# Kernel optimization log

Measured on AMD Instinct MI355X. Metric: run time of the kernel, lower is better.

## Reference

```python
import jax, jax.numpy as jnp
import numpy as np

# Static DAG configuration (mirrors GraphState): 1 input node + L layers of K nodes.
L = 8          # depth layers (well under t_budget=12)
K = 8          # nodes per layer
D = 128        # node hidden width (node.D)
B = 4096       # batch size
INDEG = 4      # in-edges per non-input node
N = 1 + L * K  # total nodes


def _build_graph():
    """Deterministic static edge lists: srcs[l][k, j] = parent node id (topologically earlier)."""
    rng = np.random.default_rng(0)
    srcs = []
    n_prev = 1  # node 0 is the INPUT node
    for _ in range(L):
        srcs.append(rng.integers(0, n_prev, size=(K, INDEG)))
        n_prev += K
    return srcs


def setup_inputs() -> dict:
    key = jax.random.key(0)
    k1, k2, k3 = jax.random.split(key, 3)
    X = jax.random.normal(k1, (B, D), dtype=jnp.float32)
    # scale ~ sqrt(2/(indeg*D)) to keep relu activations O(1) over 8 layers
    W = jax.random.normal(k2, (N, D, D), dtype=jnp.float32) * 0.06
    b = jax.random.normal(k3, (N, D), dtype=jnp.float32) * 0.01
    return {"X_batch": X, "W_all": W, "bias_all": b}


def reference(X_batch, W_all, bias_all):
    srcs = _build_graph()  # static python/numpy index constants -> jit-friendly
    # INPUT node (id 0): input_dim == D so no zero-padding; V_out = relu(X W^T + b)
    v0 = jax.nn.relu(X_batch @ W_all[0].T + bias_all[0])          # (B, D)
    outs = v0[None]                                               # (n_done, B, D)
    node = 1
    for l in range(L):
        idx = srcs[l]                                             # (K, INDEG) static
        V_in = outs[idx].sum(axis=1)                              # inbox gather-sum -> (K, B, D)
        Wl = W_all[node:node + K]                                 # (K, D, D)
        bl = bias_all[node:node + K]                              # (K, D)
        V_weighted = jnp.einsum('kbd,ked->kbe', V_in, Wl) + bl[:, None, :]
        V_out = jax.nn.relu(V_weighted)                           # apply_primitive(relu)
        outs = jnp.concatenate([outs, V_out], axis=0)
        node += K
    # output nodes = last layer; final = mean over fired output nodes
    return outs[-K:].mean(axis=0)                                 # (B, D)
```

## Files before the change

### kernel.cpp

```cpp
#include <hip/hip_runtime.h>
#include <cstdint>
#include <cstring>

#define BATCH   4096
#define DIM     128
#define NLAYERS 8
#define KNODES  8
#define NDEG    4
#define NNODES  65
#define NODE_ELEMS (BATCH * DIM)
#define ROWS    16
#define SLOTS   35
#define TILE_B  (ROWS * 256)
#define NTHREADS 512

typedef float    f32x4 __attribute__((ext_vector_type(4)));
typedef short    s16x8 __attribute__((ext_vector_type(8)));
typedef uint32_t u32x4 __attribute__((ext_vector_type(4)));

struct LayerSrcs { int p[KNODES][NDEG]; };

struct Sched {
  uint64_t pinfo[NLAYERS * KNODES];
  int8_t   dst[NLAYERS * KNODES];
  int8_t   root_dst;
};

__device__ __forceinline__ float bf_lo(uint32_t u) {
  union { uint32_t i; float f; } x; x.i = u << 16; return x.f;
}
__device__ __forceinline__ float bf_hi(uint32_t u) {
  union { uint32_t i; float f; } x; x.i = u & 0xffff0000u; return x.f;
}
__device__ __forceinline__ uint32_t f2bf(float f) {
  union { float f; uint32_t i; } x; x.f = f;
  return (x.i + 0x7fffu + ((x.i >> 16) & 1u)) >> 16;
}
__device__ __forceinline__ uint32_t pack2(float a, float b) {
  return f2bf(a) | (f2bf(b) << 16);
}

__global__ __launch_bounds__(256)
void pack_w(const float* __restrict__ W, uint16_t* __restrict__ Wp) {
  int gid  = blockIdx.x * 256 + threadIdx.x;
  int lane = gid & 63;
  int n    = (gid >> 6) & 7;
  int ks   = (gid >> 9) & 3;
  int node = gid >> 11;
  int col  = n * 16 + (lane & 15);
  int k0   = ks * 32 + (lane >> 4) * 8;
  const float* src = W + ((size_t)node * DIM + col) * DIM + k0;
  f32x4 v0 = *(const f32x4*)src;
  f32x4 v1 = *(const f32x4*)(src + 4);
  u32x4 pk;
  pk.x = pack2(v0.x, v0.y); pk.y = pack2(v0.z, v0.w);
  pk.z = pack2(v1.x, v1.y); pk.w = pack2(v1.z, v1.w);
  *(u32x4*)(Wp + (size_t)gid * 8) = pk;
}

__device__ __forceinline__ void gemm_node(
    char* lds, int sbuf, int n, int dstv,
    const uint16_t* __restrict__ Wp, const float* __restrict__ bias,
    uint16_t* __restrict__ outs, float* macc,
    int row0, int lane, int w, int lr, int lg)
{
  if (dstv == -3) return;
  const char* sb = lds + (size_t)(SLOTS + sbuf) * TILE_B;
  s16x8 af[4], wf[4];
#pragma unroll
  for (int ks = 0; ks < 4; ++ks) {
    af[ks] = *(const s16x8*)(sb + ((lr * 256 + ks * 64 + lg * 16) ^ ((lr & 7) << 4)));
    wf[ks] = *(const s16x8*)(Wp + ((((size_t)n * 4 + ks) * 8 + w) << 9) + lane * 8);
  }
  f32x4 acc = (f32x4){0.f, 0.f, 0.f, 0.f};
#pragma unroll
  for (int ks = 0; ks < 4; ++ks)
    acc = __builtin_amdgcn_mfma_f32_16x16x32_bf16(af[ks], wf[ks], acc, 0, 0, 0);

  const int col = w * 16 + lr;
  const float bv = bias[(size_t)n * DIM + col];
  if (dstv >= 0) {
    char* db = lds + (size_t)dstv * TILE_B;
#pragma unroll
    for (int j = 0; j < 4; ++j) {
      int row = lg * 4 + j;
      float v = fmaxf(acc[j] + bv, 0.f);
      *(uint16_t*)(db + ((row * 256 + col * 2) ^ ((row & 7) << 4))) = (uint16_t)f2bf(v);
    }
  } else if (dstv == -1) {
    uint16_t* gb = outs + (size_t)n * NODE_ELEMS + (size_t)row0 * DIM + col;
#pragma unroll
    for (int j = 0; j < 4; ++j) {
      int row = lg * 4 + j;
      float v = fmaxf(acc[j] + bv, 0.f);
      gb[(size_t)row * DIM] = (uint16_t)f2bf(v);
      gb += 0;
    }
  } else {
#pragma unroll
    for (int j = 0; j < 4; ++j)
      macc[j] += 0.125f * fmaxf(acc[j] + bv, 0.f);
  }
}


__device__ __forceinline__ void gemm_node2(
    char* lds, int sbuf, int n, int dstv,
    const uint16_t* __restrict__ Wp, const float* __restrict__ bias,
    uint16_t* __restrict__ outs, float* macc,
    int row0, int lane, int w, int lr, int lg)
{
  if (dstv == -3) return;
  const char* sb = lds + (size_t)(SLOTS + sbuf) * TILE_B;
  s16x8 af[4], wf[4];
#pragma unroll
  for (int ks = 0; ks < 4; ++ks) {
    af[ks] = *(const s16x8*)(sb + ((lr * 256 + ks * 64 + lg * 16) ^ ((lr & 7) << 4)));
    wf[ks] = *(const s16x8*)(Wp + ((((size_t)n * 4 + ks) * 8 + w) << 9) + lane * 8);
  }
  f32x4 acc = (f32x4){0.f, 0.f, 0.f, 0.f};
#pragma unroll
  for (int ks = 0; ks < 4; ++ks)
    acc = __builtin_amdgcn_mfma_f32_16x16x32_bf16(af[ks], wf[ks], acc, 0, 0, 0);

  const int col = w * 16 + lr;
  const float bv = bias[(size_t)n * DIM + col];
  if (dstv >= 0) {
    char* db = lds + (size_t)dstv * TILE_B;
#pragma unroll
    for (int j = 0; j < 4; ++j) {
      int row = lg * 4 + j;
      float v = fmaxf(acc[j] + bv, 0.f);
      *(uint16_t*)(db + ((row * 256 + col * 2) ^ ((row & 7) << 4))) = (uint16_t)f2bf(v);
    }
  } else if (dstv == -1) {
    uint16_t* gb = outs + (size_t)n * NODE_ELEMS + (size_t)row0 * DIM + col;
#pragma unroll
    for (int j = 0; j < 4; ++j) {
      int row = lg * 4 + j;
      float v = fmaxf(acc[j] + bv, 0.f);
      gb[(size_t)row * DIM] = (uint16_t)f2bf(v);
    }
  } else {
#pragma unroll
    for (int j = 0; j < 4; ++j)
      macc[j] += 0.125f * fmaxf(acc[j] + bv, 0.f);
  }
}

__global__ __launch_bounds__(NTHREADS)
void dag_exec(const float* __restrict__ X, const uint16_t* __restrict__ Wp,
              const float* __restrict__ bias, uint16_t* __restrict__ outs,
              float* __restrict__ out, Sched sch)
{
  __shared__ char lds[(SLOTS + 4) * TILE_B];
  const int t    = threadIdx.x;
  const int lane = t & 63;
  const int w    = t >> 6;
  const int lr   = lane & 15;
  const int lg   = lane >> 4;
  const int row0 = blockIdx.x * ROWS;

  float macc[4] = {0.f, 0.f, 0.f, 0.f};

  if (t < ROWS * 16) {
    int r = t >> 4, c = t & 15;
    const float* xp = X + (size_t)(row0 + r) * DIM + c * 8;
    f32x4 v0 = *(const f32x4*)xp;
    f32x4 v1 = *(const f32x4*)(xp + 4);
    u32x4 pk;
    pk.x = pack2(v0.x, v0.y); pk.y = pack2(v0.z, v0.w);
    pk.z = pack2(v1.x, v1.y); pk.w = pack2(v1.z, v1.w);
    int off = (r * 256 + c * 16) ^ ((r & 7) << 4);
    *(u32x4*)(lds + (size_t)SLOTS * TILE_B + off) = pk;
  }
  __syncthreads();
  gemm_node2(lds, 0, 0, sch.root_dst, Wp, bias, outs, macc, row0, lane, w, lr, lg);
  __syncthreads();

  for (int l = 0; l < NLAYERS; ++l) {
#pragma unroll
    for (int h = 0; h < 2; ++h) {
      const int k0 = h * 4;
      const uint64_t pi0 = sch.pinfo[l * KNODES + k0 + 0];
      const uint64_t pi1 = sch.pinfo[l * KNODES + k0 + 1];
      const uint64_t pi2 = sch.pinfo[l * KNODES + k0 + 2];
      const uint64_t pi3 = sch.pinfo[l * KNODES + k0 + 3];
      const int d0 = sch.dst[l * KNODES + k0 + 0];
      const int d1 = sch.dst[l * KNODES + k0 + 1];
      const int d2 = sch.dst[l * KNODES + k0 + 2];
      const int d3 = sch.dst[l * KNODES + k0 + 3];

#pragma unroll
      for (int it = 0; it < 2; ++it) {
        const int lin = it * NTHREADS + t;
        const int nk  = lin >> 8;
        const uint64_t pinfo = (nk < 2) ? (nk == 0 ? pi0 : pi1) : (nk == 2 ? pi2 : pi3);
        const int dv         = (nk < 2) ? (nk == 0 ? d0 : d1) : (nk == 2 ? d2 : d3);
        if (dv != -3) {
          const int r = (lin >> 4) & 15, c = lin & 15;
          const int linoff = r * 256 + (c << 4);
          const int soff   = linoff ^ ((r & 7) << 4);
          float s0 = 0, s1 = 0, s2 = 0, s3 = 0, s4 = 0, s5 = 0, s6 = 0, s7 = 0;
#pragma unroll
          for (int p = 0; p < NDEG; ++p) {
            const int e  = (int)((pinfo >> (p * 16)) & 0xffff);
            const int ps = (e & 0xff) - 1;
            u32x4 v;
            if (ps >= 0) {
              v = *(const u32x4*)(lds + (size_t)ps * TILE_B + soff);
            } else {
              const int pid = e >> 8;
              v = *(const u32x4*)((const char*)(outs + (size_t)pid * NODE_ELEMS +
                                                (size_t)row0 * DIM) + linoff);
            }
            s0 += bf_lo(v.x); s1 += bf_hi(v.x);
            s2 += bf_lo(v.y); s3 += bf_hi(v.y);
            s4 += bf_lo(v.z); s5 += bf_hi(v.z);
            s6 += bf_lo(v.w); s7 += bf_hi(v.w);
          }
          u32x4 pk;
          pk.x = pack2(s0, s1); pk.y = pack2(s2, s3);
          pk.z = pack2(s4, s5); pk.w = pack2(s6, s7);
          *(u32x4*)(lds + (size_t)(SLOTS + nk) * TILE_B + soff) = pk;
        }
      }
      __syncthreads();

#pragma unroll
      for (int nk = 0; nk < 4; ++nk) {
        const int dv = (nk < 2) ? (nk == 0 ? d0 : d1) : (nk == 2 ? d2 : d3);
        const int n  = 1 + l * KNODES + k0 + nk;
        gemm_node2(lds, nk, n, dv, Wp, bias, outs, macc, row0, lane, w, lr, lg);
      }
      __syncthreads();
    }
  }

  {
    const int col = w * 16 + lr;
#pragma unroll
    for (int j = 0; j < 4; ++j) {
      const int row = lg * 4 + j;
      out[(size_t)(row0 + row) * DIM + col] = macc[j];
    }
  }
}

namespace nprng {
static inline uint32_t hashmix(uint32_t v, uint32_t& hc) {
  v ^= hc; hc *= 0x931e8875u; v *= hc; v ^= v >> 16; return v;
}
static inline uint32_t mixf(uint32_t x, uint32_t y) {
  uint32_t r = x * 0xca01f9ddu - y * 0x4973f715u;
  r ^= r >> 16;
  return r;
}
struct Pcg {
  unsigned __int128 state, inc;
  bool has32; uint32_t saved;
  void step() {
    const unsigned __int128 MUL =
        ((unsigned __int128)2549297995355413924ULL << 64) | 4865540595714422341ULL;
    state = state * MUL + inc;
  }
  void init_seed0() {
    uint32_t pool[4];
    uint32_t hc = 0x43b0d7e5u;
    for (int i = 0; i < 4; ++i) pool[i] = hashmix(0u, hc);
    for (int s = 0; s < 4; ++s)
      for (int d = 0; d < 4; ++d)
        if (s != d) pool[d] = mixf(pool[d], hashmix(pool[s], hc));
    uint32_t st[8];
    uint32_t hb = 0x8b51f9ddu;
    int cyc = 0;
    for (int i = 0; i < 8; ++i) {
      uint32_t dv = pool[cyc]; cyc = (cyc + 1) & 3;
      dv ^= hb; hb *= 0x58f38dedu; dv *= hb; dv ^= dv >> 16;
      st[i] = dv;
    }
    uint64_t v[4];
    for (int i = 0; i < 4; ++i)
      v[i] = (uint64_t)st[2 * i] | ((uint64_t)st[2 * i + 1] << 32);
    unsigned __int128 s128 = ((unsigned __int128)v[0] << 64) | v[1];
    unsigned __int128 i128 = ((unsigned __int128)v[2] << 64) | v[3];
    state = 0; inc = (i128 << 1) | 1;
    step(); state += s128; step();
    has32 = false; saved = 0;
  }
  uint64_t next64() {
    step();
    uint64_t rot = (uint64_t)(state >> 122);
    uint64_t x = (uint64_t)(state >> 64) ^ (uint64_t)state;
    return rot ? ((x >> rot) | (x << (64 - rot))) : x;
  }
  uint32_t next32() {
    if (has32) { has32 = false; return saved; }
    uint64_t v = next64();
    has32 = true; saved = (uint32_t)(v >> 32);
    return (uint32_t)v;
  }
  uint32_t lemire32(uint32_t rng_incl) {
    uint32_t rng_excl = rng_incl + 1u;
    uint64_t m = (uint64_t)next32() * (uint64_t)rng_excl;
    uint32_t leftover = (uint32_t)m;
    if (leftover < rng_excl) {
      uint32_t threshold = (0xFFFFFFFFu - rng_incl) % rng_excl;
      while (leftover < threshold) {
        m = (uint64_t)next32() * (uint64_t)rng_excl;
        leftover = (uint32_t)m;
      }
    }
    return (uint32_t)(m >> 32);
  }
};
}

extern "C" void kernel_launch(void* const* d_in, const int* in_sizes, int n_in,
                              void* d_out, int out_size, void* d_ws, size_t ws_size,
                              hipStream_t stream) {
  const float* X    = (const float*)d_in[0];
  const float* W    = (const float*)d_in[1];
  const float* bias = (const float*)d_in[2];
  float* out        = (float*)d_out;

  uint16_t* Wp   = (uint16_t*)d_ws;
  uint16_t* outs = (uint16_t*)((char*)d_ws + (size_t)NNODES * DIM * DIM * 2);

  nprng::Pcg rng; rng.init_seed0();
  LayerSrcs srcs[NLAYERS];
  int n_prev = 1;
  for (int l = 0; l < NLAYERS; ++l) {
    for (int k = 0; k < KNODES; ++k)
      for (int j = 0; j < NDEG; ++j)
        srcs[l].p[k][j] = (n_prev == 1) ? 0 : (int)rng.lemire32((uint32_t)(n_prev - 1));
    n_prev += KNODES;
  }

  bool alive[NNODES];
  for (int i = 0; i < NNODES; ++i) alive[i] = false;
  for (int i = NNODES - KNODES; i < NNODES; ++i) alive[i] = true;
  for (int l = NLAYERS - 1; l >= 0; --l)
    for (int k = 0; k < KNODES; ++k)
      if (alive[1 + l * KNODES + k])
        for (int j = 0; j < NDEG; ++j) alive[srcs[l].p[k][j]] = true;

  int last_use[NNODES];
  for (int i = 0; i < NNODES; ++i) last_use[i] = -1;
  for (int l = 0; l < NLAYERS; ++l)
    for (int k = 0; k < KNODES; ++k)
      if (alive[1 + l * KNODES + k])
        for (int j = 0; j < NDEG; ++j) {
          int s = srcs[l].p[k][j];
          if (l > last_use[s]) last_use[s] = l;
        }

  int slot_of[NNODES];
  for (int i = 0; i < NNODES; ++i) slot_of[i] = -1;
  int freeStk[SLOTS], nfree = 0;
  for (int i = SLOTS - 1; i >= 0; --i) freeStk[nfree++] = i;

  Sched sch;
  slot_of[0] = freeStk[--nfree];
  sch.root_dst = (int8_t)slot_of[0];

  for (int l = 0; l < NLAYERS; ++l) {
    for (int k = 0; k < KNODES; ++k) {
      const int node = 1 + l * KNODES + k;
      int dv;
      if (!alive[node])            dv = -3;
      else if (l == NLAYERS - 1)   dv = -2;
      else if (nfree > 0)          dv = slot_of[node] = freeStk[--nfree];
      else                         dv = -1;
      sch.dst[l * KNODES + k] = (int8_t)dv;

      uint64_t w64 = 0;
      for (int j = 0; j < NDEG; ++j) {
        const int src = srcs[l].p[k][j];
        const int enc = ((slot_of[src] + 1) & 0xff) | (src << 8);
        w64 |= (uint64_t)enc << (j * 16);
      }
      sch.pinfo[l * KNODES + k] = w64;
    }
    for (int n = 0; n < NNODES; ++n)
      if (slot_of[n] >= 0 && last_use[n] == l) {
        freeStk[nfree++] = slot_of[n];
        slot_of[n] = -1;
      }
  }

  pack_w<<<dim3(520), dim3(256), 0, stream>>>(W, Wp);
  dag_exec<<<dim3(BATCH / ROWS), dim3(NTHREADS), 0, stream>>>(X, Wp, bias, outs, out, sch);
}
```

Measured before the change: 125.6 us.

## Replace inbox gather-sum with per-parent MFMA accumulation, one wave pair per node

Each layer now assigns one pair of waves to each of the 8 nodes (1024 threads) and computes all nodes of a layer concurrently. Instead of summing the parent activations into a bf16 staging buffer before the GEMM, each parent fragment is fed directly into MFMA, so the summation happens in the fp32 accumulator. This removes the staging buffers and one barrier per half-layer, and the root GEMM reads X straight into registers. The cost is 4x the MFMA count, more threads competing for registers, and LDS atomics for the output mean.

```diff
diff --git a/kernel.cpp b/kernel.cpp
--- a/kernel.cpp
+++ b/kernel.cpp
@@ -10,9 +10,9 @@
 #define NNODES  65
 #define NODE_ELEMS (BATCH * DIM)
 #define ROWS    16
-#define SLOTS   35
+#define SLOTS   37
 #define TILE_B  (ROWS * 256)
-#define NTHREADS 512
+#define NTHREADS 1024
 
 typedef float    f32x4 __attribute__((ext_vector_type(4)));
 typedef short    s16x8 __attribute__((ext_vector_type(8)));
@@ -26,12 +26,6 @@
   int8_t   root_dst;
 };
 
-__device__ __forceinline__ float bf_lo(uint32_t u) {
-  union { uint32_t i; float f; } x; x.i = u << 16; return x.f;
-}
-__device__ __forceinline__ float bf_hi(uint32_t u) {
-  union { uint32_t i; float f; } x; x.i = u & 0xffff0000u; return x.f;
-}
 __device__ __forceinline__ uint32_t f2bf(float f) {
   union { float f; uint32_t i; } x; x.f = f;
   return (x.i + 0x7fffu + ((x.i >> 16) & 1u)) >> 16;
@@ -58,192 +52,137 @@
   *(u32x4*)(Wp + (size_t)gid * 8) = pk;
 }
 
-__device__ __forceinline__ void gemm_node(
-    char* lds, int sbuf, int n, int dstv,
-    const uint16_t* __restrict__ Wp, const float* __restrict__ bias,
-    uint16_t* __restrict__ outs, float* macc,
-    int row0, int lane, int w, int lr, int lg)
-{
-  if (dstv == -3) return;
-  const char* sb = lds + (size_t)(SLOTS + sbuf) * TILE_B;
-  s16x8 af[4], wf[4];
-#pragma unroll
-  for (int ks = 0; ks < 4; ++ks) {
-    af[ks] = *(const s16x8*)(sb + ((lr * 256 + ks * 64 + lg * 16) ^ ((lr & 7) << 4)));
-    wf[ks] = *(const s16x8*)(Wp + ((((size_t)n * 4 + ks) * 8 + w) << 9) + lane * 8);
-  }
-  f32x4 acc = (f32x4){0.f, 0.f, 0.f, 0.f};
-#pragma unroll
-  for (int ks = 0; ks < 4; ++ks)
-    acc = __builtin_amdgcn_mfma_f32_16x16x32_bf16(af[ks], wf[ks], acc, 0, 0, 0);
-
-  const int col = w * 16 + lr;
-  const float bv = bias[(size_t)n * DIM + col];
-  if (dstv >= 0) {
-    char* db = lds + (size_t)dstv * TILE_B;
-#pragma unroll
-    for (int j = 0; j < 4; ++j) {
-      int row = lg * 4 + j;
-      float v = fmaxf(acc[j] + bv, 0.f);
-      *(uint16_t*)(db + ((row * 256 + col * 2) ^ ((row & 7) << 4))) = (uint16_t)f2bf(v);
-    }
-  } else if (dstv == -1) {
-    uint16_t* gb = outs + (size_t)n * NODE_ELEMS + (size_t)row0 * DIM + col;
-#pragma unroll
-    for (int j = 0; j < 4; ++j) {
-      int row = lg * 4 + j;
-      float v = fmaxf(acc[j] + bv, 0.f);
-      gb[(size_t)row * DIM] = (uint16_t)f2bf(v);
-      gb += 0;
-    }
-  } else {
-#pragma unroll
-    for (int j = 0; j < 4; ++j)
-      macc[j] += 0.125f * fmaxf(acc[j] + bv, 0.f);
-  }
-}
-
-
-__device__ __forceinline__ void gemm_node2(
-    char* lds, int sbuf, int n, int dstv,
-    const uint16_t* __restrict__ Wp, const float* __restrict__ bias,
-    uint16_t* __restrict__ outs, float* macc,
-    int row0, int lane, int w, int lr, int lg)
-{
-  if (dstv == -3) return;
-  const char* sb = lds + (size_t)(SLOTS + sbuf) * TILE_B;
-  s16x8 af[4], wf[4];
-#pragma unroll
-  for (int ks = 0; ks < 4; ++ks) {
-    af[ks] = *(const s16x8*)(sb + ((lr * 256 + ks * 64 + lg * 16) ^ ((lr & 7) << 4)));
-    wf[ks] = *(const s16x8*)(Wp + ((((size_t)n * 4 + ks) * 8 + w) << 9) + lane * 8);
-  }
-  f32x4 acc = (f32x4){0.f, 0.f, 0.f, 0.f};
-#pragma unroll
-  for (int ks = 0; ks < 4; ++ks)
-    acc = __builtin_amdgcn_mfma_f32_16x16x32_bf16(af[ks], wf[ks], acc, 0, 0, 0);
-
-  const int col = w * 16 + lr;
-  const float bv = bias[(size_t)n * DIM + col];
-  if (dstv >= 0) {
-    char* db = lds + (size_t)dstv * TILE_B;
-#pragma unroll
-    for (int j = 0; j < 4; ++j) {
-      int row = lg * 4 + j;
-      float v = fmaxf(acc[j] + bv, 0.f);
-      *(uint16_t*)(db + ((row * 256 + col * 2) ^ ((row & 7) << 4))) = (uint16_t)f2bf(v);
-    }
-  } else if (dstv == -1) {
-    uint16_t* gb = outs + (size_t)n * NODE_ELEMS + (size_t)row0 * DIM + col;
-#pragma unroll
-    for (int j = 0; j < 4; ++j) {
-      int row = lg * 4 + j;
-      float v = fmaxf(acc[j] + bv, 0.f);
-      gb[(size_t)row * DIM] = (uint16_t)f2bf(v);
-    }
-  } else {
-#pragma unroll
-    for (int j = 0; j < 4; ++j)
-      macc[j] += 0.125f * fmaxf(acc[j] + bv, 0.f);
-  }
-}
-
 __global__ __launch_bounds__(NTHREADS)
 void dag_exec(const float* __restrict__ X, const uint16_t* __restrict__ Wp,
               const float* __restrict__ bias, uint16_t* __restrict__ outs,
               float* __restrict__ out, Sched sch)
 {
-  __shared__ char lds[(SLOTS + 4) * TILE_B];
+  __shared__ char lds[SLOTS * TILE_B + 2048 * 4];
+  float* mb = (float*)(lds + (size_t)SLOTS * TILE_B);
+
   const int t    = threadIdx.x;
   const int lane = t & 63;
-  const int w    = t >> 6;
+  const int wv   = t >> 6;
   const int lr   = lane & 15;
   const int lg   = lane >> 4;
+  const int kn   = wv & 7;
+  const int h    = wv >> 3;
   const int row0 = blockIdx.x * ROWS;
 
-  float macc[4] = {0.f, 0.f, 0.f, 0.f};
-
-  if (t < ROWS * 16) {
-    int r = t >> 4, c = t & 15;
-    const float* xp = X + (size_t)(row0 + r) * DIM + c * 8;
-    f32x4 v0 = *(const f32x4*)xp;
-    f32x4 v1 = *(const f32x4*)(xp + 4);
-    u32x4 pk;
-    pk.x = pack2(v0.x, v0.y); pk.y = pack2(v0.z, v0.w);
-    pk.z = pack2(v1.x, v1.y); pk.w = pack2(v1.z, v1.w);
-    int off = (r * 256 + c * 16) ^ ((r & 7) << 4);
-    *(u32x4*)(lds + (size_t)SLOTS * TILE_B + off) = pk;
+  mb[t] = 0.f;
+  mb[t + 1024] = 0.f;
+
+  if (wv < 2) {
+    const int h2 = wv;
+    f32x4 acc[4];
+#pragma unroll
+    for (int n = 0; n < 4; ++n) acc[n] = (f32x4){0.f, 0.f, 0.f, 0.f};
+#pragma unroll
+    for (int ks = 0; ks < 4; ++ks) {
+      const float* xp = X + (size_t)(row0 + lr) * DIM + ks * 32 + lg * 8;
+      f32x4 v0 = *(const f32x4*)xp;
+      f32x4 v1 = *(const f32x4*)(xp + 4);
+      u32x4 pk;
+      pk.x = pack2(v0.x, v0.y); pk.y = pack2(v0.z, v0.w);
+      pk.z = pack2(v1.x, v1.y); pk.w = pack2(v1.z, v1.w);
+      s16x8 af;
+      __builtin_memcpy(&af, &pk, 16);
+#pragma unroll
+      for (int n = 0; n < 4; ++n) {
+        const size_t ci = ((size_t)(0 * 4 + ks) * 8 + h2 * 4 + n);
+        s16x8 wf = *(const s16x8*)(Wp + (ci << 9) + lane * 8);
+        acc[n] = __builtin_amdgcn_mfma_f32_16x16x32_bf16(af, wf, acc[n], 0, 0, 0);
+      }
+    }
+    char* db = lds + (size_t)sch.root_dst * TILE_B;
+#pragma unroll
+    for (int n = 0; n < 4; ++n) {
+      const int col = (h2 * 4 + n) * 16 + lr;
+      const float bv = bias[col];
+#pragma unroll
+      for (int j = 0; j < 4; ++j) {
+        const int row = lg * 4 + j;
+        float v = fmaxf(acc[n][j] + bv, 0.f);
+        *(uint16_t*)(db + ((row * 256 + col * 2) ^ ((row & 7) << 4))) = (uint16_t)f2bf(v);
+      }
+    }
   }
   __syncthreads();
-  gemm_node2(lds, 0, 0, sch.root_dst, Wp, bias, outs, macc, row0, lane, w, lr, lg);
-  __syncthreads();
 
   for (int l = 0; l < NLAYERS; ++l) {
-#pragma unroll
-    for (int h = 0; h < 2; ++h) {
-      const int k0 = h * 4;
-      const uint64_t pi0 = sch.pinfo[l * KNODES + k0 + 0];
-      const uint64_t pi1 = sch.pinfo[l * KNODES + k0 + 1];
-      const uint64_t pi2 = sch.pinfo[l * KNODES + k0 + 2];
-      const uint64_t pi3 = sch.pinfo[l * KNODES + k0 + 3];
-      const int d0 = sch.dst[l * KNODES + k0 + 0];
-      const int d1 = sch.dst[l * KNODES + k0 + 1];
-      const int d2 = sch.dst[l * KNODES + k0 + 2];
-      const int d3 = sch.dst[l * KNODES + k0 + 3];
-
-#pragma unroll
-      for (int it = 0; it < 2; ++it) {
-        const int lin = it * NTHREADS + t;
-        const int nk  = lin >> 8;
-        const uint64_t pinfo = (nk < 2) ? (nk == 0 ? pi0 : pi1) : (nk == 2 ? pi2 : pi3);
-        const int dv         = (nk < 2) ? (nk == 0 ? d0 : d1) : (nk == 2 ? d2 : d3);
-        if (dv != -3) {
-          const int r = (lin >> 4) & 15, c = lin & 15;
-          const int linoff = r * 256 + (c << 4);
-          const int soff   = linoff ^ ((r & 7) << 4);
-          float s0 = 0, s1 = 0, s2 = 0, s3 = 0, s4 = 0, s5 = 0, s6 = 0, s7 = 0;
-#pragma unroll
-          for (int p = 0; p < NDEG; ++p) {
-            const int e  = (int)((pinfo >> (p * 16)) & 0xffff);
-            const int ps = (e & 0xff) - 1;
-            u32x4 v;
-            if (ps >= 0) {
-              v = *(const u32x4*)(lds + (size_t)ps * TILE_B + soff);
-            } else {
-              const int pid = e >> 8;
-              v = *(const u32x4*)((const char*)(outs + (size_t)pid * NODE_ELEMS +
-                                                (size_t)row0 * DIM) + linoff);
-            }
-            s0 += bf_lo(v.x); s1 += bf_hi(v.x);
-            s2 += bf_lo(v.y); s3 += bf_hi(v.y);
-            s4 += bf_lo(v.z); s5 += bf_hi(v.z);
-            s6 += bf_lo(v.w); s7 += bf_hi(v.w);
+    const int idx  = l * KNODES + kn;
+    const int node = 1 + idx;
+    const int dv   = sch.dst[idx];
+    const uint64_t pinfo = sch.pinfo[idx];
+
+    if (dv != -3) {
+      f32x4 acc[4];
+#pragma unroll
+      for (int n = 0; n < 4; ++n) acc[n] = (f32x4){0.f, 0.f, 0.f, 0.f};
+
+#pragma unroll
+      for (int ks = 0; ks < 4; ++ks) {
+        s16x8 af[NDEG];
+#pragma unroll
+        for (int p = 0; p < NDEG; ++p) {
+          const int e  = (int)((pinfo >> (p * 16)) & 0xffff);
+          const int ps = (e & 0xff) - 1;
+          if (ps >= 0) {
+            af[p] = *(const s16x8*)(lds + (size_t)ps * TILE_B +
+                     ((lr * 256 + ks * 64 + lg * 16) ^ ((lr & 7) << 4)));
+          } else {
+            const int pid = e >> 8;
+            af[p] = *(const s16x8*)(outs + (size_t)pid * NODE_ELEMS +
+                     (size_t)(row0 + lr) * DIM + ks * 32 + lg * 8);
           }
-          u32x4 pk;
-          pk.x = pack2(s0, s1); pk.y = pack2(s2, s3);
-          pk.z = pack2(s4, s5); pk.w = pack2(s6, s7);
-          *(u32x4*)(lds + (size_t)(SLOTS + nk) * TILE_B + soff) = pk;
         }
-      }
-      __syncthreads();
-
-#pragma unroll
-      for (int nk = 0; nk < 4; ++nk) {
-        const int dv = (nk < 2) ? (nk == 0 ? d0 : d1) : (nk == 2 ? d2 : d3);
-        const int n  = 1 + l * KNODES + k0 + nk;
-        gemm_node2(lds, nk, n, dv, Wp, bias, outs, macc, row0, lane, w, lr, lg);
-      }
-      __syncthreads();
-    }
+#pragma unroll
+        for (int n = 0; n < 4; ++n) {
+          const size_t ci = ((size_t)node * 4 + ks) * 8 + h * 4 + n;
+          s16x8 wf = *(const s16x8*)(Wp + (ci << 9) + lane * 8);
+#pragma unroll
+          for (int p = 0; p < NDEG; ++p)
+            acc[n] = __builtin_amdgcn_mfma_f32_16x16x32_bf16(af[p], wf, acc[n], 0, 0, 0);
+        }
+      }
+
+#pragma unroll
+      for (int n = 0; n < 4; ++n) {
+        const int col = (h * 4 + n) * 16 + lr;
+        const float bv = bias[(size_t)node * DIM + col];
+        if (dv >= 0) {
+          char* db = lds + (size_t)dv * TILE_B;
+#pragma unroll
+          for (int j = 0; j < 4; ++j) {
+            const int row = lg * 4 + j;
+            float v = fmaxf(acc[n][j] + bv, 0.f);
+            *(uint16_t*)(db + ((row * 256 + col * 2) ^ ((row & 7) << 4))) = (uint16_t)f2bf(v);
+          }
+        } else if (dv == -1) {
+          uint16_t* gb = outs + (size_t)node * NODE_ELEMS + (size_t)row0 * DIM + col;
+#pragma unroll
+          for (int j = 0; j < 4; ++j) {
+            const int row = lg * 4 + j;
+            float v = fmaxf(acc[n][j] + bv, 0.f);
+            gb[(size_t)row * DIM] = (uint16_t)f2bf(v);
+          }
+        } else {
+#pragma unroll
+          for (int j = 0; j < 4; ++j) {
+            const int row = lg * 4 + j;
+            float v = fmaxf(acc[n][j] + bv, 0.f);
+            atomicAdd(mb + row * DIM + col, v);
+          }
+        }
+      }
+    }
+    __syncthreads();
   }
 
   {
-    const int col = w * 16 + lr;
-#pragma unroll
-    for (int j = 0; j < 4; ++j) {
-      const int row = lg * 4 + j;
-      out[(size_t)(row0 + row) * DIM + col] = macc[j];
-    }
+    const int r = t >> 7, c = t & 127;
+    out[(size_t)(row0 + r) * DIM + c]     = mb[t] * 0.125f;
+    out[(size_t)(row0 + 8 + r) * DIM + c] = mb[t + 1024] * 0.125f;
   }
 }
 
```

Result: faster. 120.9 us (-3.8%).
